# Optimization experiments

Measured on AMD Instinct MI355X. Metric: run time of the kernel, lower is better.

Reference implementation:

```python
import jax, jax.numpy as jnp
import numpy as np

B, NORM_NC, LABEL_NC, STYLE_SIZE, NHIDDEN, H, W, KS = 8, 256, 19, 512, 128, 128, 128, 3
EPS = 1e-5


def conv2d(x, w, b):
    # NCHW conv, stride 1, SAME padding (pw = ks//2)
    y = jax.lax.conv_general_dilated(x, w, window_strides=(1, 1), padding='SAME',
                                     dimension_numbers=('NCHW', 'OIHW', 'NCHW'))
    return y + b[None, :, None, None]


def setup_inputs() -> dict:
    key = jax.random.key(0)
    ks = jax.random.split(key, 16)
    s = 0.05
    return {
        'x': jax.random.normal(ks[0], (B, NORM_NC, H, W), jnp.float32),
        'segmap': jax.random.uniform(ks[1], (B, LABEL_NC, H, W), jnp.float32),
        'style': jax.random.normal(ks[2], (B, LABEL_NC, STYLE_SIZE), jnp.float32),
        'w_shared': jax.random.normal(ks[3], (NHIDDEN, LABEL_NC, KS, KS), jnp.float32) * s,
        'b_shared': jnp.zeros((NHIDDEN,), jnp.float32),
        'w_gamma': jax.random.normal(ks[4], (NORM_NC, NHIDDEN, KS, KS), jnp.float32) * s,
        'b_gamma': jnp.zeros((NORM_NC,), jnp.float32),
        'w_beta': jax.random.normal(ks[5], (NORM_NC, NHIDDEN, KS, KS), jnp.float32) * s,
        'b_beta': jnp.zeros((NORM_NC,), jnp.float32),
        'w_sgamma': jax.random.normal(ks[6], (NORM_NC, STYLE_SIZE, KS, KS), jnp.float32) * s,
        'b_sgamma': jnp.zeros((NORM_NC,), jnp.float32),
        'w_sbeta': jax.random.normal(ks[7], (NORM_NC, STYLE_SIZE, KS, KS), jnp.float32) * s,
        'b_sbeta': jnp.zeros((NORM_NC,), jnp.float32),
        'alpha_beta': jax.random.uniform(ks[8], (1,), jnp.float32),
        'alpha_gamma': jax.random.uniform(ks[9], (1,), jnp.float32),
    }


def reference(x, segmap, style, w_shared, b_shared, w_gamma, b_gamma, w_beta, b_beta,
              w_sgamma, b_sgamma, w_sbeta, b_sbeta, alpha_beta, alpha_gamma):
    # InstanceNorm2d (affine=False): per-(b,c) normalization over HxW, biased var
    mean = jnp.mean(x, axis=(2, 3), keepdims=True)
    var = jnp.var(x, axis=(2, 3), keepdims=True)
    normalized = (x - mean) * jax.lax.rsqrt(var + EPS)

    # segmap already at fm_size == out_size -> nearest interpolate is identity
    actv = jax.nn.relu(conv2d(segmap, w_shared, b_shared))  # (B, nhidden, H, W)

    # fused per-pixel contraction over label channels:
    # (style[b,l,s] * segmap[b,l,h,w]).sum(l) -> (B, style_size, H, W)
    style_map = jnp.einsum('bls,blhw->bshw', style, segmap)

    gamma = conv2d(actv, w_gamma, b_gamma)
    beta = conv2d(actv, w_beta, b_beta)
    gamma_style = conv2d(style_map, w_sgamma, b_sgamma)
    beta_style = conv2d(style_map, w_sbeta, b_sbeta)

    wb = jax.nn.sigmoid(alpha_beta)[0]
    wg = jax.nn.sigmoid(alpha_gamma)[0]
    combined_offset = wb * beta_style + (1.0 - wb) * beta
    combined_scale = wg * gamma_style + (1.0 - wg) * gamma + 1.0
    return normalized * combined_scale + combined_offset
```

## Files before the change

### kernel.cpp

```cpp
#include <hip/hip_runtime.h>
#include <hip/hip_bf16.h>
#include <cstdint>

#define B_ 8
#define LABEL_NC 19
#define H_ 128
#define W_ 128
#define UC 640
#define EPS_ 1e-5f

typedef __attribute__((ext_vector_type(8))) short s8v;
typedef __attribute__((ext_vector_type(4))) float f4v;
typedef __attribute__((ext_vector_type(4))) int i4v;
typedef unsigned short ushort_t;

__device__ __forceinline__ ushort_t f2b(float f) {
    union { float f; uint32_t u; } a; a.f = f;
    uint32_t u = a.u;
    return (ushort_t)((u + 0x7FFFu + ((u >> 16) & 1u)) >> 16);
}

__device__ __forceinline__ void gl2lds16(const ushort_t* g, ushort_t* l) {
    __builtin_amdgcn_global_load_lds(
        (const __attribute__((address_space(1))) unsigned int*)g,
        (__attribute__((address_space(3))) unsigned int*)l, 16, 0, 0);
}

__global__ void __launch_bounds__(256) k_aux(
    const float* __restrict__ x,
    const float* __restrict__ segmap, const float* __restrict__ style,
    const float* __restrict__ w_shared, const float* __restrict__ b_shared,
    const float* __restrict__ w_gamma, const float* __restrict__ w_beta,
    const float* __restrict__ w_sgamma, const float* __restrict__ w_sbeta,
    const float* __restrict__ b_gamma, const float* __restrict__ b_beta,
    const float* __restrict__ b_sgamma, const float* __restrict__ b_sbeta,
    const float* __restrict__ alpha_beta, const float* __restrict__ alpha_gamma,
    ushort_t* __restrict__ U, ushort_t* __restrict__ Wt,
    float* __restrict__ mean, float* __restrict__ rstd,
    float* __restrict__ bias_s, float* __restrict__ bias_o,
    float* __restrict__ zpage)
{
    __shared__ float seg[3][LABEL_NC][W_];
    int bid = blockIdx.x;

    if (bid < 1024) {
        int b = bid >> 7, h = bid & 127;
        const float* segb = segmap + (size_t)b * (LABEL_NC * H_ * W_);
        for (int idx = threadIdx.x; idx < 3 * LABEL_NC * W_; idx += 256) {
            int w = idx & 127;
            int l = (idx >> 7) % LABEL_NC;
            int rr = idx / (LABEL_NC * W_);
            int hh = h + rr - 1;
            seg[rr][l][w] = (hh >= 0 && hh < H_) ? segb[((size_t)l * H_ + hh) * W_ + w] : 0.f;
        }
        __syncthreads();

        int t = threadIdx.x;
        int w = t & 127;
        int grp = __builtin_amdgcn_readfirstlane(t >> 7);
        ushort_t* Urow = U + (((size_t)(b * H_ + h)) * W_ + w) * UC;

        union pack16 { ushort_t u[16]; i4v v[2]; };

        for (int cb = 0; cb < 4; ++cb) {
            int co0 = grp * 64 + cb * 16;
            float acc[16];
            #pragma unroll
            for (int i = 0; i < 16; ++i) acc[i] = b_shared[co0 + i];
            for (int l = 0; l < LABEL_NC; ++l) {
                #pragma unroll
                for (int kh = 0; kh < 3; ++kh) {
                    float sm = (w > 0)   ? seg[kh][l][w - 1] : 0.f;
                    float s0 = seg[kh][l][w];
                    float sp = (w < 127) ? seg[kh][l][w + 1] : 0.f;
                    const float* wp = w_shared + ((size_t)co0 * LABEL_NC + l) * 9 + kh * 3;
                    #pragma unroll
                    for (int i = 0; i < 16; ++i) {
                        const float* wpi = wp + i * (LABEL_NC * 9);
                        acc[i] += sm * wpi[0] + s0 * wpi[1] + sp * wpi[2];
                    }
                }
            }
            pack16 pk;
            #pragma unroll
            for (int i = 0; i < 16; ++i) pk.u[i] = f2b(acc[i] > 0.f ? acc[i] : 0.f);
            *(i4v*)(Urow + co0) = pk.v[0];
            *(i4v*)(Urow + co0 + 8) = pk.v[1];
        }

        float segr[LABEL_NC];
        #pragma unroll
        for (int l = 0; l < LABEL_NC; ++l) segr[l] = seg[1][l][w];
        const float* styb = style + (size_t)b * (LABEL_NC * 512);
        for (int sb = 0; sb < 16; ++sb) {
            int s0 = grp * 256 + sb * 16;
            float acc[16];
            #pragma unroll
            for (int i = 0; i < 16; ++i) acc[i] = 0.f;
            for (int l = 0; l < LABEL_NC; ++l) {
                const float* sp = styb + l * 512 + s0;
                float sl = segr[l];
                #pragma unroll
                for (int i = 0; i < 16; ++i) acc[i] += sl * sp[i];
            }
            pack16 pk;
            #pragma unroll
            for (int i = 0; i < 16; ++i) pk.u[i] = f2b(acc[i]);
            *(i4v*)(Urow + 128 + s0) = pk.v[0];
            *(i4v*)(Urow + 128 + s0 + 8) = pk.v[1];
        }
    } else if (bid < 3072) {
        int bc = bid - 1024;
        const float4* p = (const float4*)(x + (size_t)bc * (H_ * W_));
        float s = 0.f, s2 = 0.f;
        for (int i = threadIdx.x; i < H_ * W_ / 4; i += 256) {
            float4 v = p[i];
            s += v.x + v.y + v.z + v.w;
            s2 += v.x * v.x + v.y * v.y + v.z * v.z + v.w * v.w;
        }
        #pragma unroll
        for (int o = 32; o > 0; o >>= 1) { s += __shfl_xor(s, o); s2 += __shfl_xor(s2, o); }
        __shared__ float red[8];
        int wave = threadIdx.x >> 6, lane = threadIdx.x & 63;
        if (lane == 0) { red[wave] = s; red[wave + 4] = s2; }
        __syncthreads();
        if (threadIdx.x == 0) {
            float ts = red[0] + red[1] + red[2] + red[3];
            float t2 = red[4] + red[5] + red[6] + red[7];
            float m = ts * (1.f / 16384.f);
            float v = t2 * (1.f / 16384.f) - m * m;
            mean[bc] = m;
            rstd[bc] = rsqrtf(v + EPS_);
        }
    } else {
        float wb = 1.f / (1.f + __expf(-alpha_beta[0]));
        float wg = 1.f / (1.f + __expf(-alpha_gamma[0]));
        int gid = (bid - 3072) * 256 + threadIdx.x;
        if (gid < 256) bias_s[gid] = wg * b_sgamma[gid] + (1.f - wg) * b_gamma[gid];
        else if (gid < 512) bias_o[gid - 256] = wb * b_sbeta[gid - 256] + (1.f - wb) * b_beta[gid - 256];
        if (gid < 8192) zpage[gid] = 0.f;

        const int total = 9 * 512 * 640;
        for (int idx = gid; idx < total; idx += 2048 * 256) {
            int tap = idx / (512 * 640);
            int r = idx - tap * (512 * 640);
            int co = r / 640, ci = r - co * 640;
            int kh = tap / 3, kw = tap - kh * 3;
            float v;
            if (co < 256) {
                if (ci < 128) v = (1.f - wg) * w_gamma[((co * 128 + ci) * 3 + kh) * 3 + kw];
                else          v = wg * w_sgamma[((co * 512 + (ci - 128)) * 3 + kh) * 3 + kw];
            } else {
                int c2 = co - 256;
                if (ci < 128) v = (1.f - wb) * w_beta[((c2 * 128 + ci) * 3 + kh) * 3 + kw];
                else          v = wb * w_sbeta[((c2 * 512 + (ci - 128)) * 3 + kh) * 3 + kw];
            }
            Wt[idx] = f2b(v);
        }
    }
}

#define BK 32

__global__ void __launch_bounds__(512, 1) k_conv(
    const ushort_t* __restrict__ U, const ushort_t* __restrict__ Wt,
    const ushort_t* __restrict__ zp,
    const float* __restrict__ x, const float* __restrict__ mean, const float* __restrict__ rstd,
    const float* __restrict__ bias_s, const float* __restrict__ bias_o,
    float* __restrict__ out)
{
    int orig = blockIdx.x;
    int wg = (orig & 7) * 128 + (orig >> 3);
    int mtile = wg >> 1;
    int cohalf = wg & 1;
    int b = mtile >> 6;
    int h0 = (mtile & 63) << 1;

    extern __shared__ ushort_t smem[];

    int t = threadIdx.x;
    int wv = t >> 6, ln = t & 63;
    int wm = wv >> 1, wn = wv & 1;

    const ushort_t* Ub = U + (size_t)b * (H_ * W_ * UC);

    f4v acc[4][8] = {};

    auto stage_A = [&](int ci0, int ab) {
        ushort_t* sAb = smem + ab * 16384;
        #pragma unroll
        for (int i = 0; i < 4; ++i) {
            int issue = wv * 4 + i;
            int hh = h0 - 1 + (issue >> 3);
            int w = issue * 16 + (ln >> 2);
            int sl = (ln & 3) ^ ((w >> 1) & 3);
            const ushort_t* src = (hh >= 0 && hh < H_)
                ? Ub + ((size_t)hh * W_ + (w & 127)) * UC + ci0 + (sl << 3)
                : zp + (size_t)ln * 8;
            gl2lds16(src, sAb + (size_t)issue * 512);
        }
    };
    auto stage_B = [&](int tapX, int ci0X, int bi) {
        ushort_t* base = smem + 32768 + bi * 8192;
        #pragma unroll
        for (int j = 0; j < 2; ++j) {
            int issue = wv * 2 + j;
            int c = issue * 16 + (ln >> 2);
            int sl = (ln & 3) ^ ((c >> 1) & 3);
            int gq = (c >> 6) & 1;
            int cbase = ((c >> 7) << 6) + (c & 63);
            int co = gq * 256 + cohalf * 128 + cbase;
            const ushort_t* src = Wt + ((size_t)tapX * 512 + co) * UC + ci0X + (sl << 3);
            gl2lds16(src, base + (size_t)issue * 512);
        }
    };

    stage_A(0, 0);
    stage_B(0, 0, 0);
    stage_B(1, 0, 1);

    for (int ch = 0; ch < 20; ++ch) {
        int ci0 = ch * BK;
        ushort_t* sAb = smem + (ch & 1) * 16384;
        bool lastch = (ch == 19);
        #pragma unroll
        for (int tap = 0; tap < 9; ++tap) {
            const int dhp1 = tap / 3;
            const int dw = tap - dhp1 * 3 - 1;
            const int bi = tap % 3;
            const int bi2 = (tap + 2) % 3;

            if (tap == 8) {
                if (lastch) { asm volatile("s_waitcnt vmcnt(0)" ::: "memory"); }
                else        { asm volatile("s_waitcnt vmcnt(6)" ::: "memory"); }
            } else          { asm volatile("s_waitcnt vmcnt(2)" ::: "memory"); }
            __builtin_amdgcn_s_barrier();

            if (tap < 7)        stage_B(tap + 2, ci0, bi2);
            else if (!lastch) {
                if (tap == 7) { stage_B(0, ci0 + BK, bi2); stage_A(ci0 + BK, (ch + 1) & 1); }
                else          stage_B(1, ci0 + BK, bi2);
            }

            ushort_t* sBb = smem + 32768 + bi * 8192;
            int sd = ln >> 4;
            s8v af[4];
            #pragma unroll
            for (int mi = 0; mi < 4; ++mi) {
                int p = wm * 64 + mi * 16 + (ln & 15);
                int q = (p & 127) + dw;
                int qc = q < 0 ? 0 : (q > 127 ? 127 : q);
                int r = (p >> 7) + dhp1;
                s8v v = *(const s8v*)&sAb[(size_t)(((r * 128 + qc) << 2) + (sd ^ ((qc >> 1) & 3))) * 8];
                if (dw != 0 && (q < 0 || q > 127)) { s8v z = {}; v = z; }
                af[mi] = v;
            }
            s8v bf[8];
            #pragma unroll
            for (int ni = 0; ni < 8; ++ni) {
                int c = wn * 128 + (ni >> 2) * 64 + (ni & 3) * 16 + (ln & 15);
                bf[ni] = *(const s8v*)&sBb[(size_t)((c << 2) + (sd ^ ((c >> 1) & 3))) * 8];
            }
            __builtin_amdgcn_s_setprio(1);
            #pragma unroll
            for (int mi = 0; mi < 4; ++mi)
                #pragma unroll
                for (int ni = 0; ni < 8; ++ni)
                    acc[mi][ni] = __builtin_amdgcn_mfma_f32_16x16x32_bf16(
                        af[mi], bf[ni], acc[mi][ni], 0, 0, 0);
            __builtin_amdgcn_s_setprio(0);
        }
    }

    int bc_base = b * 256;
    #pragma unroll
    for (int ni = 0; ni < 4; ++ni) {
        int chn = cohalf * 128 + wn * 64 + ni * 16 + (ln & 15);
        float bs = bias_s[chn] + 1.f;
        float bo = bias_o[chn];
        float mu = mean[bc_base + chn];
        float rs = rstd[bc_base + chn];
        #pragma unroll
        for (int mi = 0; mi < 4; ++mi) {
            #pragma unroll
            for (int r = 0; r < 4; ++r) {
                int p = wm * 64 + mi * 16 + ((ln >> 4) << 2) + r;
                int hh = h0 + (p >> 7);
                int ww = p & 127;
                size_t xi = (((size_t)(bc_base + chn)) * H_ + hh) * W_ + ww;
                float xn = (x[xi] - mu) * rs;
                out[xi] = xn * (acc[mi][ni][r] + bs) + (acc[mi][ni + 4][r] + bo);
            }
        }
    }
}

extern "C" void kernel_launch(void* const* d_in, const int* in_sizes, int n_in,
                              void* d_out, int out_size, void* d_ws, size_t ws_size,
                              hipStream_t stream)
{
    const float* x        = (const float*)d_in[0];
    const float* segmap   = (const float*)d_in[1];
    const float* style    = (const float*)d_in[2];
    const float* w_shared = (const float*)d_in[3];
    const float* b_shared = (const float*)d_in[4];
    const float* w_gamma  = (const float*)d_in[5];
    const float* b_gamma  = (const float*)d_in[6];
    const float* w_beta   = (const float*)d_in[7];
    const float* b_beta   = (const float*)d_in[8];
    const float* w_sgamma = (const float*)d_in[9];
    const float* b_sgamma = (const float*)d_in[10];
    const float* w_sbeta  = (const float*)d_in[11];
    const float* b_sbeta  = (const float*)d_in[12];
    const float* alpha_beta  = (const float*)d_in[13];
    const float* alpha_gamma = (const float*)d_in[14];
    float* out = (float*)d_out;

    char* ws = (char*)d_ws;
    float*    ws_mean  = (float*)(ws + 0);
    float*    ws_rstd  = (float*)(ws + 8192);
    float*    ws_bs    = (float*)(ws + 16384);
    float*    ws_bo    = (float*)(ws + 18432);
    ushort_t* ws_Wt    = (ushort_t*)(ws + 20480);
    ushort_t* ws_zp    = (ushort_t*)(ws + 6 * 1024 * 1024 - 65536);
    ushort_t* ws_U     = (ushort_t*)(ws + 6 * 1024 * 1024);

    (void)hipFuncSetAttribute((const void*)k_conv,
                              hipFuncAttributeMaxDynamicSharedMemorySize, 114688);

    k_aux<<<dim3(5120), dim3(256), 0, stream>>>(x, segmap, style, w_shared, b_shared,
                                                w_gamma, w_beta, w_sgamma, w_sbeta,
                                                b_gamma, b_beta, b_sgamma, b_sbeta,
                                                alpha_beta, alpha_gamma,
                                                ws_U, ws_Wt, ws_mean, ws_rstd,
                                                ws_bs, ws_bo, (float*)ws_zp);
    k_conv<<<dim3(1024), dim3(512), 114688, stream>>>(ws_U, ws_Wt, ws_zp, x, ws_mean, ws_rstd,
                                                      ws_bs, ws_bo, out);
}
```

Baseline: 924.6 us.

## Precompute LDS fragment offsets, widen shared conv accumulators, vectorize epilogue I/O

```diff
diff --git a/kernel.cpp b/kernel.cpp
--- a/kernel.cpp
+++ b/kernel.cpp
@@ -62,30 +62,36 @@
 
         union pack16 { ushort_t u[16]; i4v v[2]; };
 
-        for (int cb = 0; cb < 4; ++cb) {
-            int co0 = grp * 64 + cb * 16;
-            float acc[16];
-            #pragma unroll
-            for (int i = 0; i < 16; ++i) acc[i] = b_shared[co0 + i];
+        {
+            float acc[64];
+            #pragma unroll
+            for (int i = 0; i < 64; ++i) acc[i] = b_shared[grp * 64 + i];
             for (int l = 0; l < LABEL_NC; ++l) {
                 #pragma unroll
                 for (int kh = 0; kh < 3; ++kh) {
                     float sm = (w > 0)   ? seg[kh][l][w - 1] : 0.f;
                     float s0 = seg[kh][l][w];
                     float sp = (w < 127) ? seg[kh][l][w + 1] : 0.f;
-                    const float* wp = w_shared + ((size_t)co0 * LABEL_NC + l) * 9 + kh * 3;
+                    const float* wp = w_shared + (((size_t)grp * 64) * LABEL_NC + l) * 9 + kh * 3;
                     #pragma unroll
-                    for (int i = 0; i < 16; ++i) {
+                    for (int i = 0; i < 64; ++i) {
                         const float* wpi = wp + i * (LABEL_NC * 9);
                         acc[i] += sm * wpi[0] + s0 * wpi[1] + sp * wpi[2];
                     }
                 }
             }
-            pack16 pk;
-            #pragma unroll
-            for (int i = 0; i < 16; ++i) pk.u[i] = f2b(acc[i] > 0.f ? acc[i] : 0.f);
-            *(i4v*)(Urow + co0) = pk.v[0];
-            *(i4v*)(Urow + co0 + 8) = pk.v[1];
+            #pragma unroll
+            for (int cb = 0; cb < 4; ++cb) {
+                pack16 pk;
+                #pragma unroll
+                for (int i = 0; i < 16; ++i) {
+                    float v = acc[cb * 16 + i];
+                    pk.u[i] = f2b(v > 0.f ? v : 0.f);
+                }
+                int co0 = grp * 64 + cb * 16;
+                *(i4v*)(Urow + co0) = pk.v[0];
+                *(i4v*)(Urow + co0 + 8) = pk.v[1];
+            }
         }
 
         float segr[LABEL_NC];
@@ -181,10 +187,31 @@
     int t = threadIdx.x;
     int wv = t >> 6, ln = t & 63;
     int wm = wv >> 1, wn = wv & 1;
+    int sd = ln >> 4;
 
     const ushort_t* Ub = U + (size_t)b * (H_ * W_ * UC);
 
     f4v acc[4][8] = {};
+
+    int aoff[3][4];
+    #pragma unroll
+    for (int dwi = 0; dwi < 3; ++dwi)
+        #pragma unroll
+        for (int mi = 0; mi < 4; ++mi) {
+            int p = wm * 64 + mi * 16 + (ln & 15);
+            int q = (p & 127) + dwi - 1;
+            int qc = q < 0 ? 0 : (q > 127 ? 127 : q);
+            int r0 = p >> 7;
+            aoff[dwi][mi] = ((r0 * 128 + qc) << 2) + (sd ^ ((qc >> 1) & 3));
+        }
+    int boff[8];
+    #pragma unroll
+    for (int ni = 0; ni < 8; ++ni) {
+        int c = wn * 128 + (ni >> 2) * 64 + (ni & 3) * 16 + (ln & 15);
+        boff[ni] = (c << 2) + (sd ^ ((c >> 1) & 3));
+    }
+    bool zlo = ((wm & 1) == 0) && ((ln & 15) == 0);
+    bool zhi = ((wm & 1) == 1) && ((ln & 15) == 15);
 
     auto stage_A = [&](int ci0, int ab) {
         ushort_t* sAb = smem + ab * 16384;
@@ -226,7 +253,7 @@
         #pragma unroll
         for (int tap = 0; tap < 9; ++tap) {
             const int dhp1 = tap / 3;
-            const int dw = tap - dhp1 * 3 - 1;
+            const int dwi = tap % 3;
             const int bi = tap % 3;
             const int bi2 = (tap + 2) % 3;
 
@@ -243,24 +270,17 @@
             }
 
             ushort_t* sBb = smem + 32768 + bi * 8192;
-            int sd = ln >> 4;
             s8v af[4];
             #pragma unroll
-            for (int mi = 0; mi < 4; ++mi) {
-                int p = wm * 64 + mi * 16 + (ln & 15);
-                int q = (p & 127) + dw;
-                int qc = q < 0 ? 0 : (q > 127 ? 127 : q);
-                int r = (p >> 7) + dhp1;
-                s8v v = *(const s8v*)&sAb[(size_t)(((r * 128 + qc) << 2) + (sd ^ ((qc >> 1) & 3))) * 8];
-                if (dw != 0 && (q < 0 || q > 127)) { s8v z = {}; v = z; }
-                af[mi] = v;
-            }
+            for (int mi = 0; mi < 4; ++mi)
+                af[mi] = *(const s8v*)&sAb[(size_t)(aoff[dwi][mi] + dhp1 * 512) * 8];
+            if (dwi == 0) { if (zlo) { s8v z = {}; af[0] = z; } }
+            if (dwi == 2) { if (zhi) { s8v z = {}; af[3] = z; } }
             s8v bf[8];
             #pragma unroll
-            for (int ni = 0; ni < 8; ++ni) {
-                int c = wn * 128 + (ni >> 2) * 64 + (ni & 3) * 16 + (ln & 15);
-                bf[ni] = *(const s8v*)&sBb[(size_t)((c << 2) + (sd ^ ((c >> 1) & 3))) * 8];
-            }
+            for (int ni = 0; ni < 8; ++ni)
+                bf[ni] = *(const s8v*)&sBb[(size_t)boff[ni] * 8];
+
             __builtin_amdgcn_s_setprio(1);
             #pragma unroll
             for (int mi = 0; mi < 4; ++mi)
@@ -282,15 +302,17 @@
         float rs = rstd[bc_base + chn];
         #pragma unroll
         for (int mi = 0; mi < 4; ++mi) {
-            #pragma unroll
-            for (int r = 0; r < 4; ++r) {
-                int p = wm * 64 + mi * 16 + ((ln >> 4) << 2) + r;
-                int hh = h0 + (p >> 7);
-                int ww = p & 127;
-                size_t xi = (((size_t)(bc_base + chn)) * H_ + hh) * W_ + ww;
-                float xn = (x[xi] - mu) * rs;
-                out[xi] = xn * (acc[mi][ni][r] + bs) + (acc[mi][ni + 4][r] + bo);
-            }
+            int p = wm * 64 + mi * 16 + ((ln >> 4) << 2);
+            int hh = h0 + (p >> 7);
+            int ww = p & 127;
+            size_t xi = (((size_t)(bc_base + chn)) * H_ + hh) * W_ + ww;
+            float4 xv = *(const float4*)&x[xi];
+            float4 ov;
+            ov.x = (xv.x - mu) * rs * (acc[mi][ni][0] + bs) + (acc[mi][ni + 4][0] + bo);
+            ov.y = (xv.y - mu) * rs * (acc[mi][ni][1] + bs) + (acc[mi][ni + 4][1] + bo);
+            ov.z = (xv.z - mu) * rs * (acc[mi][ni][2] + bs) + (acc[mi][ni + 4][2] + bo);
+            ov.w = (xv.w - mu) * rs * (acc[mi][ni][3] + bs) + (acc[mi][ni + 4][3] + bo);
+            *(float4*)&out[xi] = ov;
         }
     }
 }
```

Result: slower. 1.162 ms (+25.6%).
